# Kernel tuning notes

Hardware: AMD Instinct MI355X
Metric: run time of the kernel (lower is better)

The kernel has to match this reference:

```python
import jax, jax.numpy as jnp
import numpy as np

EPS = 1e-5  # torch BatchNorm1d default eps

def _bn(x, g, b, m, v):
    # eval-mode BatchNorm1d with running statistics
    return (x - m) * jax.lax.rsqrt(v + EPS) * g + b

def setup_inputs() -> dict:
    key = jax.random.key(0)
    ks = jax.random.split(key, 6)
    N, E, D = 10000, 320000, 128
    h = jax.random.normal(ks[0], (N, D), dtype=jnp.float32)
    src = jax.random.randint(ks[1], (E,), 0, N)
    dst = jax.random.randint(ks[2], (E,), 0, N)
    # Linear weights (torch layout: [out, in]), kaiming-ish scale
    W0 = jax.random.normal(ks[3], (128, 256), dtype=jnp.float32) * (1.0 / np.sqrt(256))
    b0 = jnp.zeros((128,), jnp.float32)
    W1 = jax.random.normal(ks[4], (128, 128), dtype=jnp.float32) * (1.0 / np.sqrt(128))
    b1 = jnp.zeros((128,), jnp.float32)
    W2 = jax.random.normal(ks[5], (1, 128), dtype=jnp.float32) * (1.0 / np.sqrt(128))
    b2 = jnp.zeros((1,), jnp.float32)
    # BatchNorm affine params + running stats per layer input size
    g0, be0, m0, v0 = jnp.ones((256,)), jnp.zeros((256,)), jnp.zeros((256,)), jnp.ones((256,))
    g1, be1, m1, v1 = jnp.ones((128,)), jnp.zeros((128,)), jnp.zeros((128,)), jnp.ones((128,))
    g2, be2, m2, v2 = jnp.ones((128,)), jnp.zeros((128,)), jnp.zeros((128,)), jnp.ones((128,))
    return dict(h=h, src=src, dst=dst, W0=W0, b0=b0, W1=W1, b1=b1, W2=W2, b2=b2,
                g0=g0, be0=be0, g1=g1, be1=be1, g2=g2, be2=be2,
                m0=m0, v0=v0, m1=m1, v1=v1, m2=m2, v2=v2)

def reference(h, src, dst, W0, b0, W1, b1, W2, b2,
              g0, be0, g1, be1, g2, be2, m0, v0, m1, v1, m2, v2):
    # edge gather + concat: [E, 2*D]
    x = jnp.concatenate([h[src], h[dst]], axis=1)
    # stage 0: BN -> Linear (dropout is identity in eval)
    x = _bn(x, g0, be0, m0, v0) @ W0.T + b0
    # stage 1: ReLU -> BN -> Linear
    x = jax.nn.relu(x)
    x = _bn(x, g1, be1, m1, v1) @ W1.T + b1
    # stage 2: ReLU -> BN -> Linear
    x = jax.nn.relu(x)
    x = _bn(x, g2, be2, m2, v2) @ W2.T + b2
    return x  # [E, 1] edge scores
```

## Files before the change

### kernel.cpp

```cpp
#include <hip/hip_runtime.h>
#include <hip/hip_bf16.h>

#define BN_EPS 1e-5f
#define MG 2

typedef short bf16x8 __attribute__((ext_vector_type(8)));
typedef float f32x4  __attribute__((ext_vector_type(4)));

static __device__ __forceinline__ unsigned short f2bf(float f) {
    union { float f; unsigned int u; } v; v.f = f;
    unsigned int u = v.u;
    unsigned int r = (u + 0x7FFFu + ((u >> 16) & 1u)) >> 16;
    return (unsigned short)r;
}

static __device__ __forceinline__ unsigned short f2bf_hw(float f) {
    __hip_bfloat16 b = __float2bfloat16(f);
    union { __hip_bfloat16 b; unsigned short u; } v; v.b = b;
    return v.u;
}

static __device__ __forceinline__ unsigned short f2h(float f) {
    union { _Float16 h; unsigned short u; } v; v.h = (_Float16)f;
    return v.u;
}

static __device__ __forceinline__ float h2f(short s) {
    union { short s; _Float16 h; } v; v.s = s;
    return (float)v.h;
}

__global__ __launch_bounds__(256) void k_prep(
        const float* __restrict__ W0, const float* __restrict__ b0,
        const float* __restrict__ W1, const float* __restrict__ b1,
        const float* __restrict__ W2, const float* __restrict__ b2,
        const float* __restrict__ g0, const float* __restrict__ be0,
        const float* __restrict__ m0, const float* __restrict__ v0,
        const float* __restrict__ g1, const float* __restrict__ be1,
        const float* __restrict__ m1, const float* __restrict__ v1,
        const float* __restrict__ g2, const float* __restrict__ be2,
        const float* __restrict__ m2, const float* __restrict__ v2,
        unsigned short* __restrict__ W0sw, unsigned short* __restrict__ W1sw,
        float* __restrict__ b0f, float* __restrict__ b1f,
        float* __restrict__ w2f, float* __restrict__ b2f) {
    int br = blockIdx.x;
    const int tid = threadIdx.x;

    if (br < 128) {
        int t = br * 256 + tid;
        int j = t & 7, lane = (t >> 3) & 63, nt = (t >> 9) & 7, kb = t >> 12;
        int k = kb * 32 + (lane >> 4) * 8 + j;
        int n = nt * 16 + (lane & 15);
        float s = g0[k] * rsqrtf(v0[k] + BN_EPS);
        W0sw[t] = f2bf(W0[n * 256 + k] * s);
        return;
    }
    br -= 128;
    if (br < 64) {
        int t = br * 256 + tid;
        int j = t & 7, lane = (t >> 3) & 63, nt = (t >> 9) & 7, kb = t >> 12;
        int k = kb * 32 + (lane >> 4) * 8 + j;
        int n = nt * 16 + (lane & 15);
        float s = g1[k] * rsqrtf(v1[k] + BN_EPS);
        W1sw[t] = f2bf(W1[n * 128 + k] * s);
        return;
    }
    br -= 64;
    {
        if (tid >= 64) return;
        const int i = br, lane = tid;
        float s0 = 0.f;
#pragma unroll
        for (int c = 0; c < 4; c++) {
            int k = c * 64 + lane;
            float sc = g0[k] * rsqrtf(v0[k] + BN_EPS);
            s0 += W0[i * 256 + k] * (be0[k] - m0[k] * sc);
        }
        float s1 = 0.f;
#pragma unroll
        for (int c = 0; c < 2; c++) {
            int k = c * 64 + lane;
            float sc = g1[k] * rsqrtf(v1[k] + BN_EPS);
            s1 += W1[i * 128 + k] * (be1[k] - m1[k] * sc);
        }
        float s2 = 0.f;
        if (i == 0) {
#pragma unroll
            for (int c = 0; c < 2; c++) {
                int k = c * 64 + lane;
                float sc = g2[k] * rsqrtf(v2[k] + BN_EPS);
                s2 += W2[k] * (be2[k] - m2[k] * sc);
            }
        }
#pragma unroll
        for (int off = 1; off < 64; off <<= 1) {
            s0 += __shfl_xor(s0, off);
            s1 += __shfl_xor(s1, off);
            s2 += __shfl_xor(s2, off);
        }
        if (lane == 0) {
            b0f[i] = b0[i] + s0;
            b1f[i] = b1[i] + s1;
            w2f[i] = W2[i] * (g2[i] * rsqrtf(v2[i] + BN_EPS));
            if (i == 0) b2f[0] = b2[0] + s2;
        }
    }
}

__global__ __launch_bounds__(256) void k_node(
        const float* __restrict__ h,
        const unsigned short* __restrict__ W0sw,
        const float* __restrict__ b0f,
        unsigned short* __restrict__ UV, int N) {
    const int tid  = threadIdx.x;
    const int wave = tid >> 6;
    const int lane = tid & 63;
    const int quad = lane >> 4;
    const int m    = lane & 15;
    const int nb   = blockIdx.x * 32;

    bf16x8 B0[8][2];
#pragma unroll
    for (int kb = 0; kb < 8; kb++)
#pragma unroll
        for (int hh = 0; hh < 2; hh++)
            B0[kb][hh] = *(const bf16x8*)(W0sw + ((kb * 8 + (wave * 2 + hh)) * 64 + lane) * 8);

    float b0v[2];
#pragma unroll
    for (int hh = 0; hh < 2; hh++) b0v[hh] = b0f[(wave * 2 + hh) * 16 + m];

    f32x4 au[MG][2], av[MG][2];
#pragma unroll
    for (int g = 0; g < MG; g++)
#pragma unroll
        for (int hh = 0; hh < 2; hh++) {
            au[g][hh] = (f32x4){0.f, 0.f, 0.f, 0.f};
            av[g][hh] = (f32x4){0.f, 0.f, 0.f, 0.f};
        }

#pragma unroll
    for (int g = 0; g < MG; g++) {
        int nrow = nb + g * 16 + m; if (nrow >= N) nrow = N - 1;
        const float* hrow = h + (size_t)nrow * 128;
#pragma unroll
        for (int kb = 0; kb < 4; kb++) {
            const float* hp = hrow + kb * 32 + quad * 8;
            f32x4 f0 = *(const f32x4*)hp;
            f32x4 f1 = *(const f32x4*)(hp + 4);
            bf16x8 a;
            a[0] = (short)f2bf_hw(f0[0]); a[1] = (short)f2bf_hw(f0[1]);
            a[2] = (short)f2bf_hw(f0[2]); a[3] = (short)f2bf_hw(f0[3]);
            a[4] = (short)f2bf_hw(f1[0]); a[5] = (short)f2bf_hw(f1[1]);
            a[6] = (short)f2bf_hw(f1[2]); a[7] = (short)f2bf_hw(f1[3]);
#pragma unroll
            for (int hh = 0; hh < 2; hh++) {
                au[g][hh] = __builtin_amdgcn_mfma_f32_16x16x32_bf16(a, B0[kb][hh],     au[g][hh], 0, 0, 0);
                av[g][hh] = __builtin_amdgcn_mfma_f32_16x16x32_bf16(a, B0[kb + 4][hh], av[g][hh], 0, 0, 0);
            }
        }
    }

#pragma unroll
    for (int g = 0; g < MG; g++)
#pragma unroll
        for (int hh = 0; hh < 2; hh++) {
            int col = (wave * 2 + hh) * 16 + m;
#pragma unroll
            for (int r = 0; r < 4; r++) {
                int node = nb + g * 16 + quad * 4 + r;
                if (node < N) {
                    UV[(size_t)node * 256 + col]       = f2h(au[g][hh][r] + b0v[hh]);
                    UV[(size_t)node * 256 + 128 + col] = f2h(av[g][hh][r]);
                }
            }
        }
}

__global__ __launch_bounds__(256, 2) void k_edge(
        const int* __restrict__ src, const int* __restrict__ dst,
        const unsigned short* __restrict__ UV,
        const unsigned short* __restrict__ W1sw,
        const float* __restrict__ b1f, const float* __restrict__ w2f,
        const float* __restrict__ b2fp,
        float* __restrict__ out, int E, int nG) {
    const int tid  = threadIdx.x;
    const int wave = tid >> 6;
    const int lane = tid & 63;
    const int q    = lane >> 4;
    const int m    = lane & 15;

    bf16x8 B1f[8][4];
#pragma unroll
    for (int nt = 0; nt < 8; nt++)
#pragma unroll
        for (int kb = 0; kb < 4; kb++)
            B1f[nt][kb] = *(const bf16x8*)(W1sw + ((kb * 8 + nt) * 64 + lane) * 8);

    float b1v[8], w2v[8];
#pragma unroll
    for (int nt = 0; nt < 8; nt++) {
        b1v[nt] = b1f[nt * 16 + m];
        w2v[nt] = w2f[nt * 16 + m];
    }
    const float b2s = *b2fp;
    const int stride = gridDim.x;

    int gi = blockIdx.x;
    bf16x8 uF[4], vF[4];
    int rsC, rdC;

    {
        int e0 = gi * 64 + wave * 16 + m; if (e0 >= E) e0 = E - 1;
        int rs0 = src[e0], rd0 = dst[e0];
#pragma unroll
        for (int kb = 0; kb < 4; kb++) {
            uF[kb] = *(const bf16x8*)(UV + (size_t)rs0 * 256 + kb * 32 + q * 8);
            vF[kb] = *(const bf16x8*)(UV + (size_t)rd0 * 256 + 128 + kb * 32 + q * 8);
        }
        int g1 = gi + stride;
        int e1 = (g1 < nG ? g1 : gi) * 64 + wave * 16 + m; if (e1 >= E) e1 = E - 1;
        rsC = src[e1]; rdC = dst[e1];
    }

    for (; gi < nG; gi += stride) {
        bf16x8 a[4];
#pragma unroll
        for (int kb = 0; kb < 4; kb++)
#pragma unroll
            for (int j = 0; j < 8; j++) {
                float s = h2f(uF[kb][j]) + h2f(vF[kb][j]);
                s = s > 0.f ? s : 0.f;
                a[kb][j] = (short)f2bf_hw(s);
            }

        {
            int rs_ = rsC, rd_ = rdC;
#pragma unroll
            for (int kb = 0; kb < 4; kb++) {
                uF[kb] = *(const bf16x8*)(UV + (size_t)rs_ * 256 + kb * 32 + q * 8);
                vF[kb] = *(const bf16x8*)(UV + (size_t)rd_ * 256 + 128 + kb * 32 + q * 8);
            }
        }
        {
            int g2 = gi + 2 * stride;
            int e2 = (g2 < nG ? g2 : gi) * 64 + wave * 16 + m; if (e2 >= E) e2 = E - 1;
            rsC = src[e2]; rdC = dst[e2];
        }

        f32x4 acc[8];
#pragma unroll
        for (int nt = 0; nt < 8; nt++) acc[nt] = (f32x4){0.f, 0.f, 0.f, 0.f};
#pragma unroll
        for (int kb = 0; kb < 4; kb++)
#pragma unroll
            for (int nt = 0; nt < 8; nt++)
                acc[nt] = __builtin_amdgcn_mfma_f32_16x16x32_bf16(a[kb], B1f[nt][kb], acc[nt], 0, 0, 0);

        float s[4] = {0.f, 0.f, 0.f, 0.f};
#pragma unroll
        for (int nt = 0; nt < 8; nt++)
#pragma unroll
            for (int r = 0; r < 4; r++) {
                float v = acc[nt][r] + b1v[nt];
                v = v > 0.f ? v : 0.f;
                s[r] += v * w2v[nt];
            }
#pragma unroll
        for (int off = 1; off < 16; off <<= 1)
#pragma unroll
            for (int r = 0; r < 4; r++) s[r] += __shfl_xor(s[r], off, 16);

        if (m == 0) {
            int eB = gi * 64 + wave * 16 + q * 4;
#pragma unroll
            for (int r = 0; r < 4; r++) {
                int e = eB + r;
                if (e < E) out[e] = s[r] + b2s;
            }
        }
    }
}

extern "C" void kernel_launch(void* const* d_in, const int* in_sizes, int n_in,
                              void* d_out, int out_size, void* d_ws, size_t ws_size,
                              hipStream_t stream) {
    const float* h   = (const float*)d_in[0];
    const int*   src = (const int*)d_in[1];
    const int*   dst = (const int*)d_in[2];
    const float* W0  = (const float*)d_in[3];
    const float* b0  = (const float*)d_in[4];
    const float* W1  = (const float*)d_in[5];
    const float* b1  = (const float*)d_in[6];
    const float* W2  = (const float*)d_in[7];
    const float* b2  = (const float*)d_in[8];
    const float* g0  = (const float*)d_in[9];
    const float* be0 = (const float*)d_in[10];
    const float* g1  = (const float*)d_in[11];
    const float* be1 = (const float*)d_in[12];
    const float* g2  = (const float*)d_in[13];
    const float* be2 = (const float*)d_in[14];
    const float* m0  = (const float*)d_in[15];
    const float* v0  = (const float*)d_in[16];
    const float* m1  = (const float*)d_in[17];
    const float* v1  = (const float*)d_in[18];
    const float* m2  = (const float*)d_in[19];
    const float* v2  = (const float*)d_in[20];
    float* out = (float*)d_out;

    const int hsz = in_sizes[0];
    const int E   = in_sizes[1];
    const int N   = hsz / 128;

    char* ws = (char*)d_ws;
    unsigned short* UV = (unsigned short*)ws;
    size_t off = ((size_t)N * 256 * 2 + 255) & ~(size_t)255;
    unsigned short* W0sw = (unsigned short*)(ws + off);  off += 65536;
    unsigned short* W1sw = (unsigned short*)(ws + off);  off += 32768;
    float* b0f = (float*)(ws + off);  off += 512;
    float* b1f = (float*)(ws + off);  off += 512;
    float* w2f = (float*)(ws + off);  off += 512;
    float* b2f = (float*)(ws + off);  off += 16;

    k_prep<<<320, 256, 0, stream>>>(W0, b0, W1, b1, W2, b2,
                                    g0, be0, m0, v0, g1, be1, m1, v1,
                                    g2, be2, m2, v2,
                                    W0sw, W1sw, b0f, b1f, w2f, b2f);

    int nodeBlocks = (N + 31) / 32;
    k_node<<<nodeBlocks, 256, 0, stream>>>(h, W0sw, b0f, UV, N);

    int nG = (E + 63) / 64;
    int nBlocks = nG < 512 ? nG : 512;
    k_edge<<<nBlocks, 256, 0, stream>>>(src, dst, UV, W1sw,
                                        b1f, w2f, b2f, out, E, nG);
}
```

Baseline: 135.0 us.

## Split edge MLP across wave pairs sharing activations via LDS to cut registers

```diff
diff --git a/kernel.cpp b/kernel.cpp
--- a/kernel.cpp
+++ b/kernel.cpp
@@ -177,107 +177,132 @@
         }
 }
 
-__global__ __launch_bounds__(256, 2) void k_edge(
+__global__ __launch_bounds__(256, 3) void k_edge(
         const int* __restrict__ src, const int* __restrict__ dst,
         const unsigned short* __restrict__ UV,
         const unsigned short* __restrict__ W1sw,
         const float* __restrict__ b1f, const float* __restrict__ w2f,
         const float* __restrict__ b2fp,
         float* __restrict__ out, int E, int nG) {
+    __shared__ __align__(16) unsigned short aS[2][2][4][64][8];
+    __shared__ float pS[2][2][2][16];
+
     const int tid  = threadIdx.x;
     const int wave = tid >> 6;
     const int lane = tid & 63;
     const int q    = lane >> 4;
     const int m    = lane & 15;
-
-    bf16x8 B1f[8][4];
-#pragma unroll
-    for (int nt = 0; nt < 8; nt++)
+    const int p2   = wave >> 1;
+    const int hf   = wave & 1;
+    const int kb0  = hf * 2;
+    const int kbp  = 2 - kb0;
+
+    bf16x8 B1h[4][4];
+#pragma unroll
+    for (int i = 0; i < 4; i++)
 #pragma unroll
         for (int kb = 0; kb < 4; kb++)
-            B1f[nt][kb] = *(const bf16x8*)(W1sw + ((kb * 8 + nt) * 64 + lane) * 8);
-
-    float b1v[8], w2v[8];
-#pragma unroll
-    for (int nt = 0; nt < 8; nt++) {
-        b1v[nt] = b1f[nt * 16 + m];
-        w2v[nt] = w2f[nt * 16 + m];
+            B1h[i][kb] = *(const bf16x8*)(W1sw + ((kb * 8 + (hf * 4 + i)) * 64 + lane) * 8);
+
+    float b1v[4], w2v[4];
+#pragma unroll
+    for (int i = 0; i < 4; i++) {
+        b1v[i] = b1f[(hf * 4 + i) * 16 + m];
+        w2v[i] = w2f[(hf * 4 + i) * 16 + m];
     }
     const float b2s = *b2fp;
     const int stride = gridDim.x;
 
     int gi = blockIdx.x;
-    bf16x8 uF[4], vF[4];
+    bf16x8 uF[2], vF[2];
     int rsC, rdC;
 
     {
-        int e0 = gi * 64 + wave * 16 + m; if (e0 >= E) e0 = E - 1;
+        int e0 = gi * 32 + p2 * 16 + m; if (e0 >= E) e0 = E - 1;
         int rs0 = src[e0], rd0 = dst[e0];
 #pragma unroll
-        for (int kb = 0; kb < 4; kb++) {
-            uF[kb] = *(const bf16x8*)(UV + (size_t)rs0 * 256 + kb * 32 + q * 8);
-            vF[kb] = *(const bf16x8*)(UV + (size_t)rd0 * 256 + 128 + kb * 32 + q * 8);
+        for (int t = 0; t < 2; t++) {
+            uF[t] = *(const bf16x8*)(UV + (size_t)rs0 * 256 + (kb0 + t) * 32 + q * 8);
+            vF[t] = *(const bf16x8*)(UV + (size_t)rd0 * 256 + 128 + (kb0 + t) * 32 + q * 8);
         }
         int g1 = gi + stride;
-        int e1 = (g1 < nG ? g1 : gi) * 64 + wave * 16 + m; if (e1 >= E) e1 = E - 1;
+        int e1 = (g1 < nG ? g1 : gi) * 32 + p2 * 16 + m; if (e1 >= E) e1 = E - 1;
         rsC = src[e1]; rdC = dst[e1];
     }
 
-    for (; gi < nG; gi += stride) {
-        bf16x8 a[4];
-#pragma unroll
-        for (int kb = 0; kb < 4; kb++)
+    int p = 0;
+    for (; gi < nG; gi += stride, p ^= 1) {
+        bf16x8 aOwn[2];
+#pragma unroll
+        for (int t = 0; t < 2; t++)
 #pragma unroll
             for (int j = 0; j < 8; j++) {
-                float s = h2f(uF[kb][j]) + h2f(vF[kb][j]);
+                float s = h2f(uF[t][j]) + h2f(vF[t][j]);
                 s = s > 0.f ? s : 0.f;
-                a[kb][j] = (short)f2bf_hw(s);
-            }
+                aOwn[t][j] = (short)f2bf_hw(s);
+            }
+        *(bf16x8*)&aS[p][p2][kb0 + 0][lane][0] = aOwn[0];
+        *(bf16x8*)&aS[p][p2][kb0 + 1][lane][0] = aOwn[1];
 
         {
             int rs_ = rsC, rd_ = rdC;
 #pragma unroll
-            for (int kb = 0; kb < 4; kb++) {
-                uF[kb] = *(const bf16x8*)(UV + (size_t)rs_ * 256 + kb * 32 + q * 8);
-                vF[kb] = *(const bf16x8*)(UV + (size_t)rd_ * 256 + 128 + kb * 32 + q * 8);
+            for (int t = 0; t < 2; t++) {
+                uF[t] = *(const bf16x8*)(UV + (size_t)rs_ * 256 + (kb0 + t) * 32 + q * 8);
+                vF[t] = *(const bf16x8*)(UV + (size_t)rd_ * 256 + 128 + (kb0 + t) * 32 + q * 8);
             }
         }
         {
             int g2 = gi + 2 * stride;
-            int e2 = (g2 < nG ? g2 : gi) * 64 + wave * 16 + m; if (e2 >= E) e2 = E - 1;
+            int e2 = (g2 < nG ? g2 : gi) * 32 + p2 * 16 + m; if (e2 >= E) e2 = E - 1;
             rsC = src[e2]; rdC = dst[e2];
         }
 
-        f32x4 acc[8];
-#pragma unroll
-        for (int nt = 0; nt < 8; nt++) acc[nt] = (f32x4){0.f, 0.f, 0.f, 0.f};
+        asm volatile("s_waitcnt lgkmcnt(0)" ::: "memory");
+        __builtin_amdgcn_s_barrier();
+        __builtin_amdgcn_sched_barrier(0);
+
+        bf16x8 a[4];
+        a[kb0]     = aOwn[0];
+        a[kb0 + 1] = aOwn[1];
+        a[kbp]     = *(const bf16x8*)&aS[p][p2][kbp][lane][0];
+        a[kbp + 1] = *(const bf16x8*)&aS[p][p2][kbp + 1][lane][0];
+
+        f32x4 acc[4];
+#pragma unroll
+        for (int i = 0; i < 4; i++) acc[i] = (f32x4){0.f, 0.f, 0.f, 0.f};
 #pragma unroll
         for (int kb = 0; kb < 4; kb++)
 #pragma unroll
-            for (int nt = 0; nt < 8; nt++)
-                acc[nt] = __builtin_amdgcn_mfma_f32_16x16x32_bf16(a[kb], B1f[nt][kb], acc[nt], 0, 0, 0);
+            for (int i = 0; i < 4; i++)
+                acc[i] = __builtin_amdgcn_mfma_f32_16x16x32_bf16(a[kb], B1h[i][kb], acc[i], 0, 0, 0);
 
         float s[4] = {0.f, 0.f, 0.f, 0.f};
 #pragma unroll
-        for (int nt = 0; nt < 8; nt++)
+        for (int i = 0; i < 4; i++)
 #pragma unroll
             for (int r = 0; r < 4; r++) {
-                float v = acc[nt][r] + b1v[nt];
+                float v = acc[i][r] + b1v[i];
                 v = v > 0.f ? v : 0.f;
-                s[r] += v * w2v[nt];
+                s[r] += v * w2v[i];
             }
 #pragma unroll
         for (int off = 1; off < 16; off <<= 1)
 #pragma unroll
             for (int r = 0; r < 4; r++) s[r] += __shfl_xor(s[r], off, 16);
-
         if (m == 0) {
-            int eB = gi * 64 + wave * 16 + q * 4;
-#pragma unroll
-            for (int r = 0; r < 4; r++) {
-                int e = eB + r;
-                if (e < E) out[e] = s[r] + b2s;
-            }
+#pragma unroll
+            for (int r = 0; r < 4; r++) pS[p][p2][hf][q * 4 + r] = s[r];
+        }
+
+        asm volatile("s_waitcnt lgkmcnt(0)" ::: "memory");
+        __builtin_amdgcn_s_barrier();
+        __builtin_amdgcn_sched_barrier(0);
+
+        if (hf == 0 && lane < 16) {
+            int e = gi * 32 + p2 * 16 + lane;
+            if (e < E)
+                out[e] = pS[p][p2][0][lane] + pS[p][p2][1][lane] + b2s;
         }
     }
 }
@@ -330,8 +355,8 @@
     int nodeBlocks = (N + 31) / 32;
     k_node<<<nodeBlocks, 256, 0, stream>>>(h, W0sw, b0f, UV, N);
 
-    int nG = (E + 63) / 64;
-    int nBlocks = nG < 512 ? nG : 512;
+    int nG = (E + 31) / 32;
+    int nBlocks = nG < 768 ? nG : 768;
     k_edge<<<nBlocks, 256, 0, stream>>>(src, dst, UV, W1sw,
                                         b1f, w2f, b2f, out, E, nG);
 }
```

After: 282.9 us. 2.1x slower.
